# Performance work log

Measured on AMD Instinct MI355X. Metric: run time of the kernel, lower is better.

Reference implementation:

```python
import jax, jax.numpy as jnp
import numpy as np

CUBE_LEN = 512
EQU_H = 1024
EQU_W = 2 * EQU_H
EQU_COUNT = 4
CHANNELS = 3


def _rodrigues(r):
    th = np.linalg.norm(r)
    if th < 1e-12:
        return np.eye(3)
    k = r / th
    K = np.array([[0.0, -k[2], k[1]], [k[2], 0.0, -k[0]], [-k[1], k[0], 0.0]])
    return np.eye(3) + np.sin(th) * K + (1.0 - np.cos(th)) * (K @ K)


def _build_lut(L, equ_h):
    # Identical math to Cube2Equirec.__init__/_intersection, fused into
    # per-pixel face id + per-pixel cube-face pixel coordinates (u, v).
    equ_w = equ_h * 2
    theta = (np.arange(equ_w) / (equ_w - 1) - 0.5) * 2 * np.pi
    phi = (np.arange(equ_h) / (equ_h - 1) - 0.5) * np.pi
    theta, phi = np.meshgrid(theta, phi)
    x = np.sin(theta) * np.cos(phi)
    y = np.sin(phi)
    z = np.cos(theta) * np.cos(phi)
    xyz = np.stack([x, y, z], axis=-1)  # [H, W, 3]
    planes = np.array([[0, 0, 1, -1], [1, 0, 0, -1], [0, 0, 1, 1],
                       [1, 0, 0, 1], [0, 1, 0, 1], [0, 1, 0, -1]], dtype=np.float64)
    r_lst = np.array([[0, 0, 0], [0, -0.5, 0], [0, 1, 0],
                      [0, 0.5, 0], [-0.5, 0, 0], [0.5, 0, 0]]) * np.pi
    f = L / 2.0
    K = np.array([[f, 0, (L - 1) / 2.0], [0, f, (L - 1) / 2.0], [0, 0, 1]])
    R_lst = np.stack([_rodrigues(r) for r in r_lst])  # [6, 3, 3]

    abc = planes[:, :3]
    with np.errstate(divide='ignore'):
        depth = -planes[:, 3][None, None, :] / (xyz @ abc.T)  # [H, W, 6]
    depth[depth < 0] = np.inf
    arg = np.argmin(depth, axis=-1)            # per-pixel face id
    dmin = np.min(depth, axis=-1)
    pts = dmin[..., None] * xyz                # intersection points
    Rs = R_lst[arg]                            # [H, W, 3, 3]
    proj = np.einsum('ij,hwjk,hwk->hwi', K, Rs, pts)  # K @ R @ pts
    uv = np.clip(proj[..., :2] / proj[..., 2:3], 0, L - 1)
    return uv.astype(np.float32), arg.astype(np.int32)


def setup_inputs() -> dict:
    key = jax.random.key(0)
    x = jax.random.normal(key, (6 * EQU_COUNT, CHANNELS, CUBE_LEN, CUBE_LEN),
                          dtype=jnp.float32)
    uv_np, face_np = _build_lut(CUBE_LEN, EQU_H)
    return {"x": x, "uv": jnp.asarray(uv_np), "face_idx": jnp.asarray(face_np)}


def _cube2equirec(x, uv, face_idx):
    # x: [6*E, C, L, L]; grid_sample(mode='bilinear', align_corners=True)
    # with grid = (uv/(L-1) - 0.5)*2 samples exactly at pixel coords uv.
    E6, C, L, _ = x.shape
    E = E6 // 6
    xr = x.reshape(E, 6, C, L, L)
    H, W = face_idx.shape
    f = face_idx.reshape(-1)                 # [N]
    u = uv[..., 0].reshape(-1)               # [N], in [0, L-1]
    v = uv[..., 1].reshape(-1)

    x0 = jnp.clip(jnp.floor(u).astype(jnp.int32), 0, L - 1)
    y0 = jnp.clip(jnp.floor(v).astype(jnp.int32), 0, L - 1)
    x1 = jnp.minimum(x0 + 1, L - 1)
    y1 = jnp.minimum(y0 + 1, L - 1)
    wx = (u - x0.astype(u.dtype))[:, None, None]  # [N,1,1]
    wy = (v - y0.astype(v.dtype))[:, None, None]

    def g(yy, xx):
        # advanced indices at axes 1,3,4 -> result [N, E, C]
        return xr[:, f, :, yy, xx]

    out = (g(y0, x0) * (1 - wx) * (1 - wy)
           + g(y0, x1) * wx * (1 - wy)
           + g(y1, x0) * (1 - wx) * wy
           + g(y1, x1) * wx * wy)              # [N, E, C]
    return jnp.transpose(out, (1, 2, 0)).reshape(E, C, H, W)


def reference(x, uv, face_idx):
    return _cube2equirec(x, uv, face_idx)
```

## Files before the change

kernel.cpp:

```cpp
#include <hip/hip_runtime.h>
#include <stdint.h>

#define CUBE_LEN   512
#define EQU_H      1024
#define EQU_W      2048
#define EQU_COUNT  4
#define CHANNELS   3
#define HW         (EQU_H * EQU_W)

typedef float f32x4 __attribute__((ext_vector_type(4)));
typedef float f32x2 __attribute__((ext_vector_type(2)));

#define IMG_OFF(i) ((uint64_t)(((i) / 3) * 18874368u + ((i) % 3) * 1048576u))

__global__ __launch_bounds__(128, 1) void cube2equirec_kernel(
    const float* __restrict__ x,
    const float* __restrict__ uv,
    const int*   __restrict__ face,
    float*       __restrict__ out)
{
    const int tid = blockIdx.x * 128 + threadIdx.x;

    const f32x4 uv4 = ((const f32x4*)uv)[tid];
    const int2  fpr = ((const int2*)face)[tid];
    const float uA = uv4.x, vA = uv4.y, uB = uv4.z, vB = uv4.w;
    const int   fA = fpr.x, fB = fpr.y;

    int x0A = (int)floorf(uA), y0A = (int)floorf(vA);
    int x0B = (int)floorf(uB), y0B = (int)floorf(vB);
    x0A = min(max(x0A, 0), 510); y0A = min(max(y0A, 0), 510);
    x0B = min(max(x0B, 0), 510); y0B = min(max(y0B, 0), 510);
    const float wxA = uA - (float)x0A, wyA = vA - (float)y0A;
    const float wxB = uB - (float)x0B, wyB = vB - (float)y0B;

    const int  xmw    = min(x0A, x0B);
    const bool compat = (fA == fB) && (y0A == y0B)
                     && ((max(x0A, x0B) - xmw) <= 2);
    const int xm = min(compat ? xmw : x0A, 508);
    const int oA = x0A - xm;
    const int oB = min(max(x0B - xm, 0), 2);

    const uint32_t vbW = (uint32_t)(fA * 3145728 + y0A * 2048 + xm * 4);
    const uint32_t vbB = (uint32_t)(fB * 3145728 + y0B * 2048 + x0B * 4);
    const uint64_t xb  = (uint64_t)x;

    const float aL = 1.f - wxA, aR = wxA;
    const float bL = 1.f - wxB, bR = wxB;
    f32x4 WA, WB;
    WA.x = (oA == 0) ? aL : 0.f;
    WA.y = (oA == 0) ? aR : ((oA == 1) ? aL : 0.f);
    WA.z = (oA == 2) ? aL : ((oA == 1) ? aR : 0.f);
    WA.w = (oA == 2) ? aR : 0.f;
    WB.x = (oB == 0) ? bL : 0.f;
    WB.y = (oB == 0) ? bR : ((oB == 1) ? bL : 0.f);
    WB.z = (oB == 2) ? bL : ((oB == 1) ? bR : 0.f);
    WB.w = (oB == 2) ? bR : 0.f;
    const f32x4 WA0 = WA * (1.f - wyA), WA1 = WA * wyA;
    const f32x4 WB0 = WB * (1.f - wyB), WB1 = WB * wyB;
    const float c00 = bL * (1.f - wyB), c01 = bR * (1.f - wyB);
    const float c10 = bL * wyB,         c11 = bR * wyB;

#define EMIT2(i, R0, R1, Q0, Q1)                                             \
    {                                                                        \
        const float ovA = R0.x * WA0.x + R0.y * WA0.y + R0.z * WA0.z         \
                        + R0.w * WA0.w + R1.x * WA1.x + R1.y * WA1.y         \
                        + R1.z * WA1.z + R1.w * WA1.w;                       \
        const float oBw = R0.x * WB0.x + R0.y * WB0.y + R0.z * WB0.z         \
                        + R0.w * WB0.w + R1.x * WB1.x + R1.y * WB1.y         \
                        + R1.z * WB1.z + R1.w * WB1.w;                       \
        const float oBf = Q0.x * c00 + Q0.y * c01 + Q1.x * c10 + Q1.y * c11; \
        f32x2 st;                                                            \
        st.x = ovA;                                                          \
        st.y = compat ? oBw : oBf;                                           \
        __builtin_nontemporal_store(st, (f32x2*)(out + (size_t)(i) * HW) + tid); \
    }

#define ROUND(I0)                                                            \
    {                                                                        \
        f32x4 r0_0, r1_0, r0_1, r1_1, r0_2, r1_2,                            \
              r0_3, r1_3, r0_4, r1_4, r0_5, r1_5;                            \
        asm volatile(                                                        \
            "global_load_dwordx4 %[a0], %[vb], %[s0]\n\t"                    \
            "global_load_dwordx4 %[b0], %[vb], %[s0] offset:2048\n\t"        \
            "global_load_dwordx4 %[a1], %[vb], %[s1]\n\t"                    \
            "global_load_dwordx4 %[b1], %[vb], %[s1] offset:2048\n\t"        \
            "global_load_dwordx4 %[a2], %[vb], %[s2]\n\t"                    \
            "global_load_dwordx4 %[b2], %[vb], %[s2] offset:2048\n\t"        \
            "global_load_dwordx4 %[a3], %[vb], %[s3]\n\t"                    \
            "global_load_dwordx4 %[b3], %[vb], %[s3] offset:2048\n\t"        \
            "global_load_dwordx4 %[a4], %[vb], %[s4]\n\t"                    \
            "global_load_dwordx4 %[b4], %[vb], %[s4] offset:2048\n\t"        \
            "global_load_dwordx4 %[a5], %[vb], %[s5]\n\t"                    \
            "global_load_dwordx4 %[b5], %[vb], %[s5] offset:2048"            \
            : [a0] "=&v"(r0_0), [b0] "=&v"(r1_0),                            \
              [a1] "=&v"(r0_1), [b1] "=&v"(r1_1),                            \
              [a2] "=&v"(r0_2), [b2] "=&v"(r1_2),                            \
              [a3] "=&v"(r0_3), [b3] "=&v"(r1_3),                            \
              [a4] "=&v"(r0_4), [b4] "=&v"(r1_4),                            \
              [a5] "=&v"(r0_5), [b5] "=&v"(r1_5)                             \
            : [vb] "v"(vbW),                                                 \
              [s0] "s"(xb + IMG_OFF((I0) + 0)),                              \
              [s1] "s"(xb + IMG_OFF((I0) + 1)),                              \
              [s2] "s"(xb + IMG_OFF((I0) + 2)),                              \
              [s3] "s"(xb + IMG_OFF((I0) + 3)),                              \
              [s4] "s"(xb + IMG_OFF((I0) + 4)),                              \
              [s5] "s"(xb + IMG_OFF((I0) + 5)));                             \
        f32x2 q0_0 = {0.f, 0.f}, q1_0 = {0.f, 0.f};                          \
        f32x2 q0_1 = {0.f, 0.f}, q1_1 = {0.f, 0.f};                          \
        f32x2 q0_2 = {0.f, 0.f}, q1_2 = {0.f, 0.f};                          \
        f32x2 q0_3 = {0.f, 0.f}, q1_3 = {0.f, 0.f};                          \
        f32x2 q0_4 = {0.f, 0.f}, q1_4 = {0.f, 0.f};                          \
        f32x2 q0_5 = {0.f, 0.f}, q1_5 = {0.f, 0.f};                          \
        if (!compat) {                                                       \
            asm volatile(                                                    \
                "global_load_dwordx2 %[a0], %[vb], %[s0]\n\t"                \
                "global_load_dwordx2 %[b0], %[vb], %[s0] offset:2048\n\t"    \
                "global_load_dwordx2 %[a1], %[vb], %[s1]\n\t"                \
                "global_load_dwordx2 %[b1], %[vb], %[s1] offset:2048\n\t"    \
                "global_load_dwordx2 %[a2], %[vb], %[s2]\n\t"                \
                "global_load_dwordx2 %[b2], %[vb], %[s2] offset:2048\n\t"    \
                "global_load_dwordx2 %[a3], %[vb], %[s3]\n\t"                \
                "global_load_dwordx2 %[b3], %[vb], %[s3] offset:2048\n\t"    \
                "global_load_dwordx2 %[a4], %[vb], %[s4]\n\t"                \
                "global_load_dwordx2 %[b4], %[vb], %[s4] offset:2048\n\t"    \
                "global_load_dwordx2 %[a5], %[vb], %[s5]\n\t"                \
                "global_load_dwordx2 %[b5], %[vb], %[s5] offset:2048"        \
                : [a0] "=&v"(q0_0), [b0] "=&v"(q1_0),                        \
                  [a1] "=&v"(q0_1), [b1] "=&v"(q1_1),                        \
                  [a2] "=&v"(q0_2), [b2] "=&v"(q1_2),                        \
                  [a3] "=&v"(q0_3), [b3] "=&v"(q1_3),                        \
                  [a4] "=&v"(q0_4), [b4] "=&v"(q1_4),                        \
                  [a5] "=&v"(q0_5), [b5] "=&v"(q1_5)                         \
                : [vb] "v"(vbB),                                             \
                  [s0] "s"(xb + IMG_OFF((I0) + 0)),                          \
                  [s1] "s"(xb + IMG_OFF((I0) + 1)),                          \
                  [s2] "s"(xb + IMG_OFF((I0) + 2)),                          \
                  [s3] "s"(xb + IMG_OFF((I0) + 3)),                          \
                  [s4] "s"(xb + IMG_OFF((I0) + 4)),                          \
                  [s5] "s"(xb + IMG_OFF((I0) + 5)));                         \
        }                                                                    \
        asm volatile("s_waitcnt vmcnt(0)" ::: "memory");                     \
        __builtin_amdgcn_sched_barrier(0);                                   \
        EMIT2((I0) + 0, r0_0, r1_0, q0_0, q1_0)                              \
        EMIT2((I0) + 1, r0_1, r1_1, q0_1, q1_1)                              \
        EMIT2((I0) + 2, r0_2, r1_2, q0_2, q1_2)                              \
        EMIT2((I0) + 3, r0_3, r1_3, q0_3, q1_3)                              \
        EMIT2((I0) + 4, r0_4, r1_4, q0_4, q1_4)                              \
        EMIT2((I0) + 5, r0_5, r1_5, q0_5, q1_5)                              \
    }

    ROUND(0)
    ROUND(6)

#undef ROUND
#undef EMIT2
}

extern "C" void kernel_launch(void* const* d_in, const int* in_sizes, int n_in,
                              void* d_out, int out_size, void* d_ws, size_t ws_size,
                              hipStream_t stream) {
    const float* x    = (const float*)d_in[0];
    const float* uv   = (const float*)d_in[1];
    const int*   face = (const int*)d_in[2];
    float*       out  = (float*)d_out;

    const int grid = (HW / 2) / 128;
    hipLaunchKernelGGL(cube2equirec_kernel, dim3(grid), dim3(128), 0, stream,
                       x, uv, face, out);
}
```

Before: 224.3 us.

## Stage cube-face source tiles in LDS for 2D output tiles

```diff
diff --git a/kernel.cpp b/kernel.cpp
--- a/kernel.cpp
+++ b/kernel.cpp
@@ -1,28 +1,47 @@
 #include <hip/hip_runtime.h>
 #include <stdint.h>
 
-#define CUBE_LEN   512
-#define EQU_H      1024
-#define EQU_W      2048
-#define EQU_COUNT  4
-#define CHANNELS   3
-#define HW         (EQU_H * EQU_W)
+#define EQU_H 1024
+#define EQU_W 2048
+#define HW (EQU_H * EQU_W)
 
 typedef float f32x4 __attribute__((ext_vector_type(4)));
 typedef float f32x2 __attribute__((ext_vector_type(2)));
 
-#define IMG_OFF(i) ((uint64_t)(((i) / 3) * 18874368u + ((i) % 3) * 1048576u))
-
-__global__ __launch_bounds__(128, 1) void cube2equirec_kernel(
+#define IMG_OFF(i)  ((uint64_t)(((i) / 3) * 18874368u + ((i) % 3) * 1048576u))
+#define IMG_FOFF(i) (((i) / 3) * 4718592 + ((i) % 3) * 262144)
+
+__device__ __forceinline__ int wave_min(int v) {
+#pragma unroll
+    for (int o = 32; o; o >>= 1) v = min(v, __shfl_xor(v, o));
+    return v;
+}
+__device__ __forceinline__ int wave_max(int v) {
+#pragma unroll
+    for (int o = 32; o; o >>= 1) v = max(v, __shfl_xor(v, o));
+    return v;
+}
+
+__global__ __launch_bounds__(256, 1) void cube2equirec_kernel(
     const float* __restrict__ x,
     const float* __restrict__ uv,
     const int*   __restrict__ face,
     float*       __restrict__ out)
 {
-    const int tid = blockIdx.x * 128 + threadIdx.x;
-
-    const f32x4 uv4 = ((const f32x4*)uv)[tid];
-    const int2  fpr = ((const int2*)face)[tid];
+    __shared__ float slds[3][2048];
+    __shared__ int   sred[24];
+
+    const int tx = blockIdx.x & 63;
+    const int ty = blockIdx.x >> 6;
+    const int pr = threadIdx.x & 15;
+    const int rw = threadIdx.x >> 4;
+    const int w  = tx * 32 + pr * 2;
+    const int h  = ty * 16 + rw;
+    const int idx  = h * EQU_W + w;
+    const int pidx = idx >> 1;
+
+    const f32x4 uv4 = ((const f32x4*)uv)[pidx];
+    const int2  fpr = ((const int2*)face)[pidx];
     const float uA = uv4.x, vA = uv4.y, uB = uv4.z, vB = uv4.w;
     const int   fA = fpr.x, fB = fpr.y;
 
@@ -33,28 +52,100 @@
     const float wxA = uA - (float)x0A, wyA = vA - (float)y0A;
     const float wxB = uB - (float)x0B, wyB = vB - (float)y0B;
 
+    int fmn = min(fA, fB),   fmx = max(fA, fB);
+    int xmn = min(x0A, x0B), xmx = max(x0A, x0B);
+    int ymn = min(y0A, y0B), ymx = max(y0A, y0B);
+    fmn = wave_min(fmn); fmx = wave_max(fmx);
+    xmn = wave_min(xmn); xmx = wave_max(xmx);
+    ymn = wave_min(ymn); ymx = wave_max(ymx);
+    const int wid = threadIdx.x >> 6, lane = threadIdx.x & 63;
+    if (lane == 0) {
+        int* p = &sred[wid * 6];
+        p[0] = fmn; p[1] = fmx; p[2] = xmn; p[3] = xmx; p[4] = ymn; p[5] = ymx;
+    }
+    __syncthreads();
+#pragma unroll
+    for (int ww = 0; ww < 4; ++ww) {
+        const int* p = &sred[ww * 6];
+        fmn = min(fmn, p[0]); fmx = max(fmx, p[1]);
+        xmn = min(xmn, p[2]); xmx = max(xmx, p[3]);
+        ymn = min(ymn, p[4]); ymx = max(ymx, p[5]);
+    }
+
+    const int  xs     = min(xmn & ~3, 448);
+    const bool staged = (fmn == fmx) && ((xmx + 1 - xs) <= 63)
+                                     && ((ymx - ymn) <= 29);
+    const uint64_t xb = (uint64_t)x;
+
+    if (staged) {
+        const int R  = ymx + 2 - ymn;
+        const int nu = R << 4;
+        const float w00A = (1.f - wxA) * (1.f - wyA), w01A = wxA * (1.f - wyA);
+        const float w10A = (1.f - wxA) * wyA,         w11A = wxA * wyA;
+        const float w00B = (1.f - wxB) * (1.f - wyB), w01B = wxB * (1.f - wyB);
+        const float w10B = (1.f - wxB) * wyB,         w11B = wxB * wyB;
+        const int lA = ((y0A - ymn) << 6) + (x0A - xs);
+        const int lB = ((y0B - ymn) << 6) + (x0B - xs);
+        const int fbase = fmn * 786432;
+
+#pragma unroll
+        for (int k = 0; k < 4; ++k) {
+#pragma unroll
+            for (int r = 0; r < 3; ++r) {
+                const float* src = x + IMG_FOFF(k * 3 + r) + fbase;
+                int u = threadIdx.x;
+                if (u < nu) {
+                    const int row = u >> 4, c4 = (u & 15) << 2;
+                    *((f32x4*)&slds[r][(row << 6) + c4]) =
+                        *(const f32x4*)(src + (ymn + row) * 512 + xs + c4);
+                }
+                u += 256;
+                if (u < nu) {
+                    const int row = u >> 4, c4 = (u & 15) << 2;
+                    *((f32x4*)&slds[r][(row << 6) + c4]) =
+                        *(const f32x4*)(src + (ymn + row) * 512 + xs + c4);
+                }
+            }
+            __syncthreads();
+#pragma unroll
+            for (int r = 0; r < 3; ++r) {
+                const int i = k * 3 + r;
+                const float* L = slds[r];
+                const float a00 = L[lA], a01 = L[lA + 1];
+                const float a10 = L[lA + 64], a11 = L[lA + 65];
+                const float b00 = L[lB], b01 = L[lB + 1];
+                const float b10 = L[lB + 64], b11 = L[lB + 65];
+                f32x2 st;
+                st.x = a00 * w00A + a01 * w01A + a10 * w10A + a11 * w11A;
+                st.y = b00 * w00B + b01 * w01B + b10 * w10B + b11 * w11B;
+                __builtin_nontemporal_store(st, (f32x2*)(out + (size_t)i * HW) + pidx);
+            }
+            __syncthreads();
+        }
+        return;
+    }
+
     const int  xmw    = min(x0A, x0B);
     const bool compat = (fA == fB) && (y0A == y0B)
                      && ((max(x0A, x0B) - xmw) <= 2);
-    const int xm = min(compat ? xmw : x0A, 508);
-    const int oA = x0A - xm;
-    const int oB = min(max(x0B - xm, 0), 2);
+    const int xm  = min(compat ? xmw : x0A, 508);
+    const int oAw = x0A - xm;
+    const int oBw = min(max(x0B - xm, 0), 2);
 
     const uint32_t vbW = (uint32_t)(fA * 3145728 + y0A * 2048 + xm * 4);
     const uint32_t vbB = (uint32_t)(fB * 3145728 + y0B * 2048 + x0B * 4);
-    const uint64_t xb  = (uint64_t)x;
 
     const float aL = 1.f - wxA, aR = wxA;
     const float bL = 1.f - wxB, bR = wxB;
     f32x4 WA, WB;
-    WA.x = (oA == 0) ? aL : 0.f;
-    WA.y = (oA == 0) ? aR : ((oA == 1) ? aL : 0.f);
-    WA.z = (oA == 2) ? aL : ((oA == 1) ? aR : 0.f);
-    WA.w = (oA == 2) ? aR : 0.f;
-    WB.x = (oB == 0) ? bL : 0.f;
-    WB.y = (oB == 0) ? bR : ((oB == 1) ? bL : 0.f);
-    WB.z = (oB == 2) ? bL : ((oB == 1) ? bR : 0.f);
-    WB.w = (oB == 2) ? bR : 0.f;
+    WA.x = (oAw == 0) ? aL : 0.f;
+    WA.y = (oAw == 0) ? aR : ((oAw == 1) ? aL : 0.f);
+    WA.z = (oAw == 2) ? aL : ((oAw == 1) ? aR : 0.f);
+    WA.w = (oAw == 2) ? aR : 0.f;
+    WB.x = (oBw == 0) ? bL : 0.f;
+    WB.y = (oBw == 0) ? bR : ((oBw == 1) ? bL : 0.f);
+    WB.z = (oBw == 2) ? bL : ((oBw == 1) ? bR : 0.f);
+    WB.w = (oBw == 2) ? bR : 0.f;
     const f32x4 WA0 = WA * (1.f - wyA), WA1 = WA * wyA;
     const f32x4 WB0 = WB * (1.f - wyB), WB1 = WB * wyB;
     const float c00 = bL * (1.f - wyB), c01 = bR * (1.f - wyB);
@@ -65,14 +156,14 @@
         const float ovA = R0.x * WA0.x + R0.y * WA0.y + R0.z * WA0.z         \
                         + R0.w * WA0.w + R1.x * WA1.x + R1.y * WA1.y         \
                         + R1.z * WA1.z + R1.w * WA1.w;                       \
-        const float oBw = R0.x * WB0.x + R0.y * WB0.y + R0.z * WB0.z         \
+        const float oBw2 = R0.x * WB0.x + R0.y * WB0.y + R0.z * WB0.z        \
                         + R0.w * WB0.w + R1.x * WB1.x + R1.y * WB1.y         \
                         + R1.z * WB1.z + R1.w * WB1.w;                       \
         const float oBf = Q0.x * c00 + Q0.y * c01 + Q1.x * c10 + Q1.y * c11; \
         f32x2 st;                                                            \
         st.x = ovA;                                                          \
-        st.y = compat ? oBw : oBf;                                           \
-        __builtin_nontemporal_store(st, (f32x2*)(out + (size_t)(i) * HW) + tid); \
+        st.y = compat ? oBw2 : oBf;                                          \
+        __builtin_nontemporal_store(st, (f32x2*)(out + (size_t)(i) * HW) + pidx); \
     }
 
 #define ROUND(I0)                                                            \
@@ -164,7 +255,7 @@
     const int*   face = (const int*)d_in[2];
     float*       out  = (float*)d_out;
 
-    const int grid = (HW / 2) / 128;
-    hipLaunchKernelGGL(cube2equirec_kernel, dim3(grid), dim3(128), 0, stream,
+    const int grid = 64 * 64;
+    hipLaunchKernelGGL(cube2equirec_kernel, dim3(grid), dim3(256), 0, stream,
                        x, uv, face, out);
 }
```

New measurement: 217.2 us. 1.03x faster.
